# Optimization experiments

Measured on AMD Instinct MI355X. Metric: run time of the kernel, lower is better.

The kernel has to match this reference:

```python
import jax, jax.numpy as jnp
import numpy as np

N_HEAD = 8
D_HEAD = 16
D_MODEL = 128
LEN_Q = 256
MEM_LEN = 256
BATCH = 4


def setup_inputs() -> dict:
    key = jax.random.key(0)
    k1, k2, k3, k4, k5 = jax.random.split(key, 5)
    h = jax.random.normal(k1, (LEN_Q, BATCH, D_MODEL), dtype=jnp.float32)
    mems = jax.random.normal(k2, (MEM_LEN, BATCH, D_MODEL), dtype=jnp.float32)
    # nn.Linear weights are [out_features, in_features]
    Wq = jax.random.normal(k3, (N_HEAD * D_HEAD, D_MODEL), dtype=jnp.float32) / np.sqrt(D_MODEL)
    Wk = jax.random.normal(k4, (N_HEAD * D_HEAD, D_MODEL), dtype=jnp.float32) / np.sqrt(D_MODEL)
    paramR = jax.random.normal(k5, (N_HEAD,), dtype=jnp.float32)
    return {"h": h, "mems": mems, "Wq": Wq, "Wk": Wk, "paramR": paramR}


def reference(h, mems, Wq, Wk, paramR):
    # h: [Lq, B, Dm], mems: [M, B, Dm]
    c = jnp.concatenate([mems, h], axis=0)  # [Lk, B, Dm]
    Lq, B = h.shape[0], h.shape[1]
    Lk = c.shape[0]
    # Linear (no bias): x @ W.T, then split heads and move to [H, B, L, Dh]
    head_q = (h @ Wq.T).reshape(Lq, B, N_HEAD, D_HEAD).transpose(2, 1, 0, 3)
    head_k = (c @ Wk.T).reshape(Lk, B, N_HEAD, D_HEAD).transpose(2, 1, 0, 3)
    # Pairwise difference: [H, B, Lq, Lk, Dh]
    diff = head_q[:, :, :, None, :] - head_k[:, :, None, :, :]
    scaled = diff * paramR[:, None, None, None, None] / jnp.pi
    # torch.sinc == jnp.sinc (normalized sinc, sinc(0)=1)
    score = jnp.abs(jnp.prod(jnp.sinc(scaled), axis=4))  # [H, B, Lq, Lk]
    # permute(2, 3, 1, 0) -> [Lq, Lk, B, H]
    return score.transpose(2, 3, 1, 0)
```

## Files before the change

### kernel.cpp

```cpp
#include <hip/hip_runtime.h>
#include <math.h>

#define LQ 256
#define MEML 256
#define LK 512
#define BB 4
#define NH 8
#define DM 128

#define IT 4

constexpr float INV2PI = 0.15915494309189535f;

__global__ __launch_bounds__(128) void proj_kernel(
    const float* __restrict__ hh, const float* __restrict__ mems,
    const float* __restrict__ Wq, const float* __restrict__ Wk,
    const float* __restrict__ paramR,
    float* __restrict__ qsP, float* __restrict__ ksT)
{
    __shared__ float x[8 * 128];
    const int blk = blockIdx.x;
    const int t = threadIdx.x;
    const bool isQ = (blk < 128);
    const int row0 = isQ ? blk * 8 : (blk - 128) * 8;
    const float* __restrict__ W = isQ ? Wq : Wk;

    for (int r = 0; r < 8; ++r) {
        const int row = row0 + r;
        const float* src = isQ ? (hh + row * DM)
                               : ((row < MEML * BB) ? (mems + row * DM)
                                                    : (hh + (row - MEML * BB) * DM));
        x[r * 128 + t] = src[t];
    }
    __syncthreads();

    float acc[8] = {0, 0, 0, 0, 0, 0, 0, 0};
    const float* wrow = W + t * DM;
    for (int k = 0; k < DM; k += 4) {
        const float4 w = *(const float4*)(wrow + k);
        #pragma unroll
        for (int r = 0; r < 8; ++r) {
            acc[r] += x[r * 128 + k + 0] * w.x + x[r * 128 + k + 1] * w.y
                    + x[r * 128 + k + 2] * w.z + x[r * 128 + k + 3] * w.w;
        }
    }
    const int h = t >> 4, d = t & 15;
    const float rs = paramR[h] * INV2PI;
    #pragma unroll
    for (int r = 0; r < 8; ++r) {
        const int row = row0 + r;
        const int b = row & 3;
        const float v = acc[r] * rs;
        if (isQ) {
            const int i = row >> 2;
            qsP[((d >> 2) * LQ + i) * 128 + (b * 8 + h) * 4 + (d & 3)] = v;
        } else {
            const int j = row >> 2;
            ksT[((d >> 2) * LK + j) * 128 + (b * 8 + h) * 4 + (d & 3)] = v;
        }
    }
}

__global__ __launch_bounds__(256, 8) void score_kernel(
    const float* __restrict__ qsP, const float* __restrict__ ksT,
    float* __restrict__ out)
{
    const int t = threadIdx.x;
    const int bh = t & 31;
    const int js = t >> 5;
    const int i0 = blockIdx.x * IT;
    const int j = blockIdx.y * 8 + js;

    constexpr float i2 = INV2PI * INV2PI;
    constexpr float i4 = i2 * i2;
    constexpr float i8 = i4 * i4;
    constexpr float C16 = i8 * i8;
    constexpr float EPS = 2.0e-4f * INV2PI;

    float k[16];
    #pragma unroll
    for (int s = 0; s < 4; ++s) {
        const float4 v = *(const float4*)(ksT + (s * LK + j) * 128 + bh * 4);
        k[s * 4 + 0] = v.x; k[s * 4 + 1] = v.y;
        k[s * 4 + 2] = v.z; k[s * 4 + 3] = v.w;
    }

    #pragma unroll 2
    for (int ii = 0; ii < IT; ++ii) {
        const int i = i0 + ii;
        float4 qv[4];
        #pragma unroll
        for (int s = 0; s < 4; ++s)
            qv[s] = *(const float4*)(qsP + (s * LQ + i) * 128 + bh * 4);

        float pn0 = 1.f, pd0 = 1.f, pn1 = 1.f, pd1 = 1.f;
        #pragma unroll
        for (int s = 0; s < 4; ++s) {
            const float qq[4] = {qv[s].x, qv[s].y, qv[s].z, qv[s].w};
            #pragma unroll
            for (int dd = 0; dd < 4; ++dd) {
                const float u2 = fmaxf(__builtin_fabsf(qq[dd] - k[s * 4 + dd]), EPS);
                const float sn = __builtin_amdgcn_sinf(u2);
                if (s < 2) { pn0 *= sn; pd0 *= u2; }
                else       { pn1 *= sn; pd1 *= u2; }
            }
        }
        const float r0 = pn0 * __builtin_amdgcn_rcpf(pd0);
        const float r1 = pn1 * __builtin_amdgcn_rcpf(pd1);
        out[(i * LK + j) * 32 + bh] = __builtin_fabsf(r0 * r1) * C16;
    }
}

extern "C" void kernel_launch(void* const* d_in, const int* in_sizes, int n_in,
                              void* d_out, int out_size, void* d_ws, size_t ws_size,
                              hipStream_t stream) {
    const float* hh     = (const float*)d_in[0];
    const float* mems   = (const float*)d_in[1];
    const float* Wq     = (const float*)d_in[2];
    const float* Wk     = (const float*)d_in[3];
    const float* paramR = (const float*)d_in[4];
    float* out = (float*)d_out;

    float* qsP = (float*)d_ws;
    float* ksT = qsP + LQ * BB * DM;

    proj_kernel<<<384, 128, 0, stream>>>(hh, mems, Wq, Wk, paramR, qsP, ksT);
    score_kernel<<<dim3(LQ / IT, LK / 8), 256, 0, stream>>>(qsP, ksT, out);
}
```

Before: 34.28 us.

## Precompute sin/cos of projections and use angle-difference identity in score

The projection kernel now also computes sin and cos of each scaled q and k value, and the score kernel evaluates sin(q-k) as sin q cos k - cos q sin k instead of calling a sine per pair. Q rows with their sin and cos are staged in shared memory per block, and each thread keeps k values, sines and cosines in registers. This swaps a transcendental per element pair for a multiply and an FMA, but triples the k loads, raises register pressure (launch bound occupancy hint lowered from 8 to 4), and may lose accuracy when q and k are close, because the difference of products cancels.

```diff
diff --git a/kernel.cpp b/kernel.cpp
--- a/kernel.cpp
+++ b/kernel.cpp
@@ -16,7 +16,8 @@
     const float* __restrict__ hh, const float* __restrict__ mems,
     const float* __restrict__ Wq, const float* __restrict__ Wk,
     const float* __restrict__ paramR,
-    float* __restrict__ qsP, float* __restrict__ ksT)
+    float* __restrict__ qT,
+    float* __restrict__ kTv, float* __restrict__ kTs, float* __restrict__ kTc)
 {
     __shared__ float x[8 * 128];
     const int blk = blockIdx.x;
@@ -51,20 +52,27 @@
         const int row = row0 + r;
         const int b = row & 3;
         const float v = acc[r] * rs;
+        const float sn = __builtin_amdgcn_sinf(v);
+        const float cs = __builtin_amdgcn_cosf(v);
         if (isQ) {
             const int i = row >> 2;
-            qsP[((d >> 2) * LQ + i) * 128 + (b * 8 + h) * 4 + (d & 3)] = v;
+            float* qp = qT + (i * 32 + b * 8 + h) * 48;
+            qp[d] = v; qp[16 + d] = sn; qp[32 + d] = cs;
         } else {
             const int j = row >> 2;
-            ksT[((d >> 2) * LK + j) * 128 + (b * 8 + h) * 4 + (d & 3)] = v;
+            const int idx = ((d >> 2) * LK + j) * 128 + (b * 8 + h) * 4 + (d & 3);
+            kTv[idx] = v; kTs[idx] = sn; kTc[idx] = cs;
         }
     }
 }
 
-__global__ __launch_bounds__(256, 8) void score_kernel(
-    const float* __restrict__ qsP, const float* __restrict__ ksT,
+__global__ __launch_bounds__(256, 4) void score_kernel(
+    const float* __restrict__ qT,
+    const float* __restrict__ kTv, const float* __restrict__ kTs,
+    const float* __restrict__ kTc,
     float* __restrict__ out)
 {
+    __shared__ float qt[IT * 32 * 48];
     const int t = threadIdx.x;
     const int bh = t & 31;
     const int js = t >> 5;
@@ -77,37 +85,56 @@
     constexpr float C16 = i8 * i8;
     constexpr float EPS = 2.0e-4f * INV2PI;
 
-    float k[16];
+    {
+        const float* src = qT + i0 * 32 * 48;
+        #pragma unroll
+        for (int rep = 0; rep < 6; ++rep) {
+            const int c4 = rep * 256 + t;
+            *(float4*)(&qt[c4 * 4]) = *(const float4*)(src + c4 * 4);
+        }
+    }
+
+    float kv[16], ks[16], kc[16];
     #pragma unroll
     for (int s = 0; s < 4; ++s) {
-        const float4 v = *(const float4*)(ksT + (s * LK + j) * 128 + bh * 4);
-        k[s * 4 + 0] = v.x; k[s * 4 + 1] = v.y;
-        k[s * 4 + 2] = v.z; k[s * 4 + 3] = v.w;
+        const int off = (s * LK + j) * 128 + bh * 4;
+        const float4 a = *(const float4*)(kTv + off);
+        const float4 b = *(const float4*)(kTs + off);
+        const float4 c = *(const float4*)(kTc + off);
+        kv[s*4+0] = a.x; kv[s*4+1] = a.y; kv[s*4+2] = a.z; kv[s*4+3] = a.w;
+        ks[s*4+0] = b.x; ks[s*4+1] = b.y; ks[s*4+2] = b.z; ks[s*4+3] = b.w;
+        kc[s*4+0] = c.x; kc[s*4+1] = c.y; kc[s*4+2] = c.z; kc[s*4+3] = c.w;
     }
+    __syncthreads();
 
-    #pragma unroll 2
+    #pragma unroll
     for (int ii = 0; ii < IT; ++ii) {
-        const int i = i0 + ii;
-        float4 qv[4];
+        const float* qrow = &qt[(ii * 32 + bh) * 48];
+        float qv[16], qs_[16], qc_[16];
         #pragma unroll
-        for (int s = 0; s < 4; ++s)
-            qv[s] = *(const float4*)(qsP + (s * LQ + i) * 128 + bh * 4);
-
+        for (int s = 0; s < 4; ++s) {
+            const float4 a = *(const float4*)(qrow + s * 4);
+            const float4 b = *(const float4*)(qrow + 16 + s * 4);
+            const float4 c = *(const float4*)(qrow + 32 + s * 4);
+            qv[s*4+0] = a.x; qv[s*4+1] = a.y; qv[s*4+2] = a.z; qv[s*4+3] = a.w;
+            qs_[s*4+0] = b.x; qs_[s*4+1] = b.y; qs_[s*4+2] = b.z; qs_[s*4+3] = b.w;
+            qc_[s*4+0] = c.x; qc_[s*4+1] = c.y; qc_[s*4+2] = c.z; qc_[s*4+3] = c.w;
+        }
         float pn0 = 1.f, pd0 = 1.f, pn1 = 1.f, pd1 = 1.f;
         #pragma unroll
-        for (int s = 0; s < 4; ++s) {
-            const float qq[4] = {qv[s].x, qv[s].y, qv[s].z, qv[s].w};
-            #pragma unroll
-            for (int dd = 0; dd < 4; ++dd) {
-                const float u2 = fmaxf(__builtin_fabsf(qq[dd] - k[s * 4 + dd]), EPS);
-                const float sn = __builtin_amdgcn_sinf(u2);
-                if (s < 2) { pn0 *= sn; pd0 *= u2; }
-                else       { pn1 *= sn; pd1 *= u2; }
-            }
+        for (int d = 0; d < 16; ++d) {
+            const float dl  = qv[d] - kv[d];
+            const float m1  = qc_[d] * ks[d];
+            const float num = __builtin_fmaf(qs_[d], kc[d], -m1);
+            const bool  g   = __builtin_fabsf(dl) > EPS;
+            const float nn  = g ? num : 1.0f;
+            const float dd  = g ? dl : INV2PI;
+            if (d < 8) { pn0 *= nn; pd0 *= dd; }
+            else       { pn1 *= nn; pd1 *= dd; }
         }
         const float r0 = pn0 * __builtin_amdgcn_rcpf(pd0);
         const float r1 = pn1 * __builtin_amdgcn_rcpf(pd1);
-        out[(i * LK + j) * 32 + bh] = __builtin_fabsf(r0 * r1) * C16;
+        out[((i0 + ii) * LK + j) * 32 + bh] = __builtin_fabsf(r0 * r1) * C16;
     }
 }
 
@@ -121,9 +148,12 @@
     const float* paramR = (const float*)d_in[4];
     float* out = (float*)d_out;
 
-    float* qsP = (float*)d_ws;
-    float* ksT = qsP + LQ * BB * DM;
+    float* qT  = (float*)d_ws;
+    float* kTv = qT  + LQ * BB * NH * 48;
+    float* kTs = kTv + LK * BB * DM;
+    float* kTc = kTs + LK * BB * DM;
 
-    proj_kernel<<<384, 128, 0, stream>>>(hh, mems, Wq, Wk, paramR, qsP, ksT);
-    score_kernel<<<dim3(LQ / IT, LK / 8), 256, 0, stream>>>(qsP, ksT, out);
+    proj_kernel<<<384, 128, 0, stream>>>(hh, mems, Wq, Wk, paramR,
+                                         qT, kTv, kTs, kTc);
+    score_kernel<<<dim3(LQ / IT, LK / 8), 256, 0, stream>>>(qT, kTv, kTs, kTc, out);
 }
```

Result: slower. 47.59 us (+38.8%).
